# Optimization experiments

Measured on AMD Instinct MI355X. Metric: run time of the kernel, lower is better.

The kernel has to match this reference:

```python
import jax, jax.numpy as jnp
import numpy as np

B, N, DIM, H, DH = 2, 2048, 1024, 16, 64
INNER = H * DH


def _rotate_half(t):
    # interleaved pairs: (..., d) -> rotate each (x1, x2) pair to (-x2, x1)
    t = t.reshape(*t.shape[:-1], -1, 2)
    x1, x2 = t[..., 0], t[..., 1]
    return jnp.stack((-x2, x1), axis=-1).reshape(*t.shape[:-2], -1)


def _apply_rotary(freqs, t):
    # freqs: [B, N, DH] -> broadcast over heads; t: [B, H, N, DH]
    f = freqs[:, None, :, :]
    return t * jnp.cos(f) + _rotate_half(t) * jnp.sin(f)


def _layernorm(x, g, b, eps=1e-5):
    mu = jnp.mean(x, axis=-1, keepdims=True)
    var = jnp.mean((x - mu) ** 2, axis=-1, keepdims=True)
    return (x - mu) * jax.lax.rsqrt(var + eps) * g + b


def setup_inputs() -> dict:
    key = jax.random.key(0)
    ks = jax.random.split(key, 8)
    x = jax.random.normal(ks[0], (B, N, DIM), jnp.float32)
    rotary = jax.random.normal(ks[1], (B, N, DH), jnp.float32)
    ln_g = jnp.ones((DIM,), jnp.float32)
    ln_b = jnp.zeros((DIM,), jnp.float32)
    w_qkv = jax.random.normal(ks[2], (DIM, 3 * INNER), jnp.float32) / np.sqrt(DIM)
    b_qkv = jnp.zeros((3 * INNER,), jnp.float32)
    w_out = jax.random.normal(ks[3], (INNER, DIM), jnp.float32) / np.sqrt(INNER)
    b_out = jnp.zeros((DIM,), jnp.float32)
    return {"x": x, "rotary": rotary, "ln_g": ln_g, "ln_b": ln_b,
            "w_qkv": w_qkv, "b_qkv": b_qkv, "w_out": w_out, "b_out": b_out}


def reference(x, rotary, ln_g, ln_b, w_qkv, b_qkv, w_out, b_out):
    h = _layernorm(x, ln_g, ln_b)
    qkv = h @ w_qkv + b_qkv                      # [B, N, 3*INNER]
    q, k, v = jnp.split(qkv, 3, axis=-1)
    # b n (h d) -> b h n d
    def to_heads(t):
        return t.reshape(B, N, H, DH).transpose(0, 2, 1, 3)
    q, k, v = to_heads(q), to_heads(k), to_heads(v)
    q = _apply_rotary(rotary, q)
    k = _apply_rotary(rotary, k)
    v = _apply_rotary(rotary, v)                 # rotate_value=True
    scale = DH ** (-0.5)
    attn = jnp.einsum('bhnd,bhmd->bhnm', q, k) * scale
    attn = jax.nn.softmax(attn, axis=-1)
    out = jnp.einsum('bhnm,bhmd->bhnd', attn, v)
    out = _apply_rotary(-rotary, out)            # inverse rotation on values
    out = out.transpose(0, 2, 1, 3).reshape(B, N, INNER)
    return out @ w_out + b_out
```

## Files before the change

kernel.cpp:

```cpp
#include <hip/hip_runtime.h>
#include <hip/hip_bf16.h>

typedef _Float16 f16;
typedef __attribute__((ext_vector_type(4))) float f32x4;
typedef __attribute__((ext_vector_type(8))) _Float16 f16x8;
typedef __attribute__((ext_vector_type(4))) _Float16 f16x4;
typedef __attribute__((ext_vector_type(2))) __fp16 hf2;

#define Bv 2
#define Nv 2048
#define DIMv 1024
#define Hv 16
#define DHv 64
#define INNERv 1024
#define QKV3v 3072

__device__ __forceinline__ void gload16(const void* g, void* l) {
  __builtin_amdgcn_global_load_lds(
      (const __attribute__((address_space(1))) void*)g,
      (__attribute__((address_space(3))) void*)l, 16, 0, 0);
}

__global__ __launch_bounds__(256) void ln_kernel(
    const float* __restrict__ x, const float* __restrict__ g,
    const float* __restrict__ bb, f16* __restrict__ h) {
  const int row = blockIdx.x;
  const int t = threadIdx.x;
  const float4 v = reinterpret_cast<const float4*>(x + (size_t)row * DIMv)[t];
  float s = v.x + v.y + v.z + v.w;
  float sq = v.x * v.x + v.y * v.y + v.z * v.z + v.w * v.w;
#pragma unroll
  for (int o = 32; o > 0; o >>= 1) {
    s += __shfl_down(s, o);
    sq += __shfl_down(sq, o);
  }
  __shared__ float red[8];
  __shared__ float musr[2];
  const int wave = t >> 6, lane = t & 63;
  if (lane == 0) { red[wave] = s; red[4 + wave] = sq; }
  __syncthreads();
  if (t == 0) {
    const float S = red[0] + red[1] + red[2] + red[3];
    const float SQ = red[4] + red[5] + red[6] + red[7];
    const float mu = S * (1.0f / DIMv);
    const float var = SQ * (1.0f / DIMv) - mu * mu;
    musr[0] = mu;
    musr[1] = rsqrtf(var + 1e-5f);
  }
  __syncthreads();
  const float mu = musr[0], rs = musr[1];
  const float4 gv = reinterpret_cast<const float4*>(g)[t];
  const float4 bv = reinterpret_cast<const float4*>(bb)[t];
  f16x4 o;
  o.x = (f16)((v.x - mu) * rs * gv.x + bv.x);
  o.y = (f16)((v.y - mu) * rs * gv.y + bv.y);
  o.z = (f16)((v.z - mu) * rs * gv.z + bv.z);
  o.w = (f16)((v.w - mu) * rs * gv.w + bv.w);
  *reinterpret_cast<f16x4*>(&h[(size_t)row * DIMv + t * 4]) = o;
}

__global__ __launch_bounds__(256) void rotcs_kernel(
    const float* __restrict__ rot, float* __restrict__ c,
    float* __restrict__ s, int n) {
  const int i = blockIdx.x * blockDim.x + threadIdx.x;
  if (i < n) {
    const float f = rot[i];
    c[i] = cosf(f);
    s[i] = sinf(f);
  }
}

__global__ __launch_bounds__(256) void transpose_f16(
    const float* __restrict__ W, f16* __restrict__ Wt, int K, int N) {
  __shared__ float tile[64][65];
  const int t = threadIdx.x;
  const int n0 = blockIdx.x * 64, k0 = blockIdx.y * 64;
#pragma unroll
  for (int i = 0; i < 16; ++i) {
    const int idx = t + i * 256;
    const int r = idx >> 6, c = idx & 63;
    tile[r][c] = W[(size_t)(k0 + r) * N + n0 + c];
  }
  __syncthreads();
#pragma unroll
  for (int i = 0; i < 16; ++i) {
    const int idx = t + i * 256;
    const int r = idx >> 6, c = idx & 63;
    Wt[(size_t)(n0 + r) * K + k0 + c] = (f16)tile[c][r];
  }
}

template <int EPI>
__global__ __launch_bounds__(256) void gemm_mfma(
    const f16* __restrict__ A, const f16* __restrict__ Bt,
    const float* __restrict__ bias, void* __restrict__ Cout,
    const float* __restrict__ cs, const float* __restrict__ sn,
    int M, int N, int K) {
  __shared__ __align__(16) f16 Asb[2][128 * 32];
  __shared__ __align__(16) f16 Bsb[2][128 * 32];
  const int t = threadIdx.x;
  const int l = t & 63, w = t >> 6;
  const int wr = w >> 1, wc = w & 1;
  const int row0 = blockIdx.y * 128, col0 = blockIdx.x * 128;

  const int i1 = t, i2 = t + 256;
  const f16* ga1 = &A[(size_t)(row0 + (i1 >> 2)) * K + (i1 & 3) * 8];
  const f16* ga2 = &A[(size_t)(row0 + (i2 >> 2)) * K + (i2 & 3) * 8];
  const f16* gb1 = &Bt[(size_t)(col0 + (i1 >> 2)) * K + (i1 & 3) * 8];
  const f16* gb2 = &Bt[(size_t)(col0 + (i2 >> 2)) * K + (i2 & 3) * 8];
  const int a_off1 = w * 512, a_off2 = w * 512 + 2048;

  const int rl = l & 15, kg = l >> 4;
  const int ar = (wr * 64 + rl) * 32 + kg * 8;
  const int br = (wc * 64 + rl) * 32 + kg * 8;

  const f32x4 zero = {0.f, 0.f, 0.f, 0.f};
  f32x4 acc[4][4];
#pragma unroll
  for (int m = 0; m < 4; ++m)
#pragma unroll
    for (int n = 0; n < 4; ++n) acc[m][n] = zero;

#define GSTAGE(buf, kk)                           \
  {                                               \
    gload16(ga1 + (kk)*32, &Asb[buf][a_off1]);    \
    gload16(ga2 + (kk)*32, &Asb[buf][a_off2]);    \
    gload16(gb1 + (kk)*32, &Bsb[buf][a_off1]);    \
    gload16(gb2 + (kk)*32, &Bsb[buf][a_off2]);    \
  }

  const int nt = K >> 5;
  GSTAGE(0, 0);

  for (int kt = 0; kt < nt; ++kt) {
    const int cur = kt & 1;
    if (kt + 1 < nt) {
      GSTAGE(cur ^ 1, kt + 1);
      asm volatile("s_waitcnt vmcnt(4)" ::: "memory");
    } else {
      asm volatile("s_waitcnt vmcnt(0)" ::: "memory");
    }
    __builtin_amdgcn_s_barrier();
    __builtin_amdgcn_sched_barrier(0);
    f16x8 af[4], bf[4];
#pragma unroll
    for (int m = 0; m < 4; ++m)
      af[m] = *reinterpret_cast<const f16x8*>(&Asb[cur][ar + m * 16 * 32]);
#pragma unroll
    for (int n = 0; n < 4; ++n)
      bf[n] = *reinterpret_cast<const f16x8*>(&Bsb[cur][br + n * 16 * 32]);
#pragma unroll
    for (int m = 0; m < 4; ++m)
#pragma unroll
      for (int n = 0; n < 4; ++n)
        acc[m][n] =
            __builtin_amdgcn_mfma_f32_16x16x32_f16(af[m], bf[n], acc[m][n], 0, 0, 0);
    asm volatile("" ::: "memory");
    __builtin_amdgcn_s_barrier();
    __builtin_amdgcn_sched_barrier(0);
  }
#undef GSTAGE

#pragma unroll
  for (int m = 0; m < 4; ++m) {
#pragma unroll
    for (int n = 0; n < 4; ++n) {
#pragma unroll
      for (int jr = 0; jr < 4; ++jr) {
        const int rg = row0 + wr * 64 + m * 16 + kg * 4 + jr;
        const int cg = col0 + wc * 64 + n * 16 + rl;
        const float v = acc[m][n][jr] + bias[cg];
        if (EPI == 0) {
          ((float*)Cout)[(size_t)rg * N + cg] = v;
        } else {
          const float p = __shfl_xor(v, 1);
          const size_t cb = (size_t)rg * DHv + (cg & 63);
          const float cc = cs[cb], ss = sn[cb];
          const float y = (l & 1) ? (v * cc + p * ss) : (v * cc - p * ss);
          ((f16*)Cout)[(size_t)rg * N + cg] = (f16)y;
        }
      }
    }
  }
}

__global__ __launch_bounds__(256) void transpose_v(
    const f16* __restrict__ qkvf, f16* __restrict__ vT) {
  const int nt = blockIdx.x, hh = blockIdx.y, b = blockIdx.z;
  const int t = threadIdx.x;
  __shared__ __align__(16) f16 tile[64][80];
  const int nl = t >> 3, dc = (t & 7) * 8;
#pragma unroll
  for (int half = 0; half < 2; ++half) {
    const int n = nl + half * 32;
    *reinterpret_cast<f16x8*>(&tile[n][dc]) = *reinterpret_cast<const f16x8*>(
        &qkvf[(size_t)(b * Nv + nt * 64 + n) * QKV3v + 2 * INNERv + hh * DHv + dc]);
  }
  __syncthreads();
  const int c0 = (t & 7) * 8;
  const int kwp = c0 >> 5, kgp = (c0 >> 3) & 3;
#pragma unroll
  for (int half = 0; half < 2; ++half) {
    const int d = (t >> 3) + half * 32;
    union { f16 e[8]; f16x8 v; } uo;
#pragma unroll
    for (int j = 0; j < 8; ++j) {
      const int mk = (j >> 2) & 1, jr = j & 3;
      const int kap = kwp * 32 + mk * 16 + kgp * 4 + jr;
      uo.e[j] = tile[kap][d];
    }
    *reinterpret_cast<f16x8*>(
        &vT[((size_t)((b * Hv + hh) * DHv + d)) * Nv + nt * 64 + c0]) = uo.v;
  }
}

__global__ __launch_bounds__(256, 4) void attn_mfma(
    const f16* __restrict__ qkvf, const f16* __restrict__ vT,
    const float* __restrict__ cs, const float* __restrict__ sn,
    f16* __restrict__ ao) {
  const int wg = blockIdx.x;
  const int swz = (wg & 7) * 128 + (wg >> 3);
  const int qb = swz & 31;
  const int hh = (swz >> 5) & 15;
  const int b = swz >> 9;
  const int t = threadIdx.x, l = t & 63, w = t >> 6;
  const int qw = w >> 1, kw = w & 1;
  const int rl = l & 15, kg = l >> 4;

  __shared__ __align__(16) f16 KsB[2][64 * 64];
  __shared__ __align__(16) f16 VtB[2][64 * 64];
  __shared__ float Lbuf[2][2][32];

  const size_t qrow0 = (size_t)(b * Nv + qb * 64 + qw * 32);
  f16x8 bq[2][2];
#pragma unroll
  for (int nq = 0; nq < 2; ++nq)
#pragma unroll
    for (int ks = 0; ks < 2; ++ks)
      bq[nq][ks] = *reinterpret_cast<const f16x8*>(
          &qkvf[(qrow0 + nq * 16 + rl) * QKV3v + hh * DHv + ks * 32 + kg * 8]);

  const f32x4 zero = {0.f, 0.f, 0.f, 0.f};
  f32x4 o_acc[2][4];
  float l_part[2] = {0.f, 0.f};
#pragma unroll
  for (int nq = 0; nq < 2; ++nq)
#pragma unroll
    for (int m2 = 0; m2 < 4; ++m2) o_acc[nq][m2] = zero;

  const int srow = t >> 3, sc0 = (t & 7) * 8;
  const f16* vtbh = vT + (size_t)((b * Hv + hh) * DHv) * Nv;
  f16x8 kr0, kr1, vr0, vr1;

#define LOADKV(tile)                                                           \
  {                                                                            \
    const size_t kb0 =                                                         \
        (size_t)(b * Nv + (tile)*64 + srow) * QKV3v + INNERv + hh * DHv + sc0; \
    kr0 = *reinterpret_cast<const f16x8*>(&qkvf[kb0]);                         \
    kr1 = *reinterpret_cast<const f16x8*>(&qkvf[kb0 + (size_t)32 * QKV3v]);    \
    const size_t vb0 = (size_t)srow * Nv + (tile)*64 + sc0;                    \
    vr0 = *reinterpret_cast<const f16x8*>(&vtbh[vb0]);                         \
    vr1 = *reinterpret_cast<const f16x8*>(&vtbh[vb0 + (size_t)32 * Nv]);       \
  }
#define STOREKV(buf)                                                           \
  {                                                                            \
    const int r1 = srow + 32;                                                  \
    *reinterpret_cast<f16x8*>(                                                 \
        &KsB[buf][(srow << 6) | (sc0 ^ ((srow & 7) << 3))]) = kr0;             \
    *reinterpret_cast<f16x8*>(                                                 \
        &KsB[buf][(r1 << 6) | (sc0 ^ ((r1 & 7) << 3))]) = kr1;                 \
    *reinterpret_cast<f16x8*>(                                                 \
        &VtB[buf][(srow << 6) | (sc0 ^ ((srow & 7) << 3))]) = vr0;             \
    *reinterpret_cast<f16x8*>(                                                 \
        &VtB[buf][(r1 << 6) | (sc0 ^ ((r1 & 7) << 3))]) = vr1;                 \
  }

  LOADKV(0);
  STOREKV(0);
  LOADKV(1);
  __syncthreads();

  const float SC2 = 0.125f * 1.44269504f;

  for (int kt = 0; kt < 32; ++kt) {
    const int cur = kt & 1;
    const f16* Kc = &KsB[cur][0];
    const f16* Vc = &VtB[cur][0];

    f16x8 ak[2][2];
#pragma unroll
    for (int mk = 0; mk < 2; ++mk)
#pragma unroll
      for (int ks = 0; ks < 2; ++ks)
        ak[mk][ks] = *reinterpret_cast<const f16x8*>(
            &Kc[((kw * 32 + mk * 16 + rl) << 6) |
                ((ks * 32 + kg * 8) ^ ((rl & 7) << 3))]);
    f16x8 av[4];
#pragma unroll
    for (int m2 = 0; m2 < 4; ++m2)
      av[m2] = *reinterpret_cast<const f16x8*>(
          &Vc[((m2 * 16 + rl) << 6) |
              ((kw * 32 + kg * 8) ^ ((rl & 7) << 3))]);

    f32x4 sa[2][2];
#pragma unroll
    for (int mk = 0; mk < 2; ++mk)
#pragma unroll
      for (int nq = 0; nq < 2; ++nq) sa[mk][nq] = zero;
    __builtin_amdgcn_s_setprio(1);
#pragma unroll
    for (int ks = 0; ks < 2; ++ks)
#pragma unroll
      for (int mk = 0; mk < 2; ++mk)
#pragma unroll
        for (int nq = 0; nq < 2; ++nq)
          sa[mk][nq] = __builtin_amdgcn_mfma_f32_16x16x32_f16(
              ak[mk][ks], bq[nq][ks], sa[mk][nq], 0, 0, 0);
    __builtin_amdgcn_s_setprio(0);

    f16x8 pb[2];
#pragma unroll
    for (int nq = 0; nq < 2; ++nq) {
      float p00 = exp2f(fminf(sa[0][nq][0] * SC2, 13.0f));
      float p01 = exp2f(fminf(sa[0][nq][1] * SC2, 13.0f));
      float p02 = exp2f(fminf(sa[0][nq][2] * SC2, 13.0f));
      float p03 = exp2f(fminf(sa[0][nq][3] * SC2, 13.0f));
      float p10 = exp2f(fminf(sa[1][nq][0] * SC2, 13.0f));
      float p11 = exp2f(fminf(sa[1][nq][1] * SC2, 13.0f));
      float p12 = exp2f(fminf(sa[1][nq][2] * SC2, 13.0f));
      float p13 = exp2f(fminf(sa[1][nq][3] * SC2, 13.0f));
      l_part[nq] += ((p00 + p01) + (p02 + p03)) + ((p10 + p11) + (p12 + p13));
      union { hf2 h2[4]; f16x8 v; } u;
      u.h2[0] = __builtin_amdgcn_cvt_pkrtz(p00, p01);
      u.h2[1] = __builtin_amdgcn_cvt_pkrtz(p02, p03);
      u.h2[2] = __builtin_amdgcn_cvt_pkrtz(p10, p11);
      u.h2[3] = __builtin_amdgcn_cvt_pkrtz(p12, p13);
      pb[nq] = u.v;
    }

    __builtin_amdgcn_s_setprio(1);
#pragma unroll
    for (int nq = 0; nq < 2; ++nq)
#pragma unroll
      for (int m2 = 0; m2 < 4; ++m2)
        o_acc[nq][m2] = __builtin_amdgcn_mfma_f32_16x16x32_f16(
            av[m2], pb[nq], o_acc[nq][m2], 0, 0, 0);
    __builtin_amdgcn_s_setprio(0);

    if (kt < 31) STOREKV(1 - cur);
    if (kt < 30) LOADKV(kt + 2);
    __syncthreads();
  }

#pragma unroll
  for (int nq = 0; nq < 2; ++nq) {
    l_part[nq] += __shfl_xor(l_part[nq], 16);
    l_part[nq] += __shfl_xor(l_part[nq], 32);
  }
  if (kg == 0) {
    Lbuf[qw][kw][rl] = l_part[0];
    Lbuf[qw][kw][16 + rl] = l_part[1];
  }
  {
    char* ob = (qw == 0 ? (char*)KsB : (char*)VtB) + kw * 8192;
#pragma unroll
    for (int nq = 0; nq < 2; ++nq)
#pragma unroll
      for (int m2 = 0; m2 < 4; ++m2)
        *reinterpret_cast<f32x4*>(
            ob + (nq * 16 + rl) * 256 +
            ((m2 * 64 + kg * 16) ^ ((rl & 7) << 4))) = o_acc[nq][m2];
  }
  __syncthreads();
  {
    const int q_local = w * 16 + (l >> 2);
    const int qw_r = q_local >> 5, q_in = q_local & 31;
    const int d0 = (l & 3) * 16;
    char* rb = (qw_r == 0 ? (char*)KsB : (char*)VtB);
    const float linv = 1.0f / (Lbuf[qw_r][0][q_in] + Lbuf[qw_r][1][q_in]);
    const size_t nq_g = (size_t)(b * Nv + qb * 64 + q_local);
    const size_t cb = nq_g * DHv + d0;
    union { f16 e[16]; f16x8 v[2]; } uo;
#pragma unroll
    for (int j = 0; j < 4; ++j) {
      const unsigned off = q_in * 256 + (((l & 3) * 64 + j * 16) ^ ((q_in & 7) << 4));
      const f32x4 a = *reinterpret_cast<const f32x4*>(rb + off);
      const f32x4 c2 = *reinterpret_cast<const f32x4*>(rb + 8192 + off);
      const float4 csv = *reinterpret_cast<const float4*>(&cs[cb + j * 4]);
      const float4 snv = *reinterpret_cast<const float4*>(&sn[cb + j * 4]);
      const float o0 = (a[0] + c2[0]) * linv;
      const float o1 = (a[1] + c2[1]) * linv;
      const float o2 = (a[2] + c2[2]) * linv;
      const float o3 = (a[3] + c2[3]) * linv;
      uo.e[j * 4 + 0] = (f16)(o0 * csv.x + o1 * snv.x);
      uo.e[j * 4 + 1] = (f16)(o1 * csv.y - o0 * snv.y);
      uo.e[j * 4 + 2] = (f16)(o2 * csv.z + o3 * snv.z);
      uo.e[j * 4 + 3] = (f16)(o3 * csv.w - o2 * snv.w);
    }
    f16* aop = &ao[nq_g * INNERv + hh * DHv + d0];
    *reinterpret_cast<f16x8*>(aop) = uo.v[0];
    *reinterpret_cast<f16x8*>(aop + 8) = uo.v[1];
  }
#undef LOADKV
#undef STOREKV
}

extern "C" void kernel_launch(void* const* d_in, const int* in_sizes, int n_in,
                              void* d_out, int out_size, void* d_ws, size_t ws_size,
                              hipStream_t stream) {
  (void)in_sizes; (void)n_in; (void)out_size; (void)ws_size;
  const float* x = (const float*)d_in[0];
  const float* rot = (const float*)d_in[1];
  const float* ln_g = (const float*)d_in[2];
  const float* ln_b = (const float*)d_in[3];
  const float* w_qkv = (const float*)d_in[4];
  const float* b_qkv = (const float*)d_in[5];
  const float* w_out = (const float*)d_in[6];
  const float* b_out = (const float*)d_in[7];

  char* p = (char*)d_ws;
  f16* h = (f16*)p;            p += (size_t)Bv * Nv * DIMv * 2;
  float* cs = (float*)p;       p += (size_t)Bv * Nv * DHv * 4;
  float* sn = (float*)p;       p += (size_t)Bv * Nv * DHv * 4;
  f16* wqT = (f16*)p;          p += (size_t)QKV3v * DIMv * 2;
  f16* woT = (f16*)p;          p += (size_t)DIMv * INNERv * 2;
  f16* qkvf = (f16*)p;         p += (size_t)Bv * Nv * QKV3v * 2;
  f16* ao = (f16*)p;           p += (size_t)Bv * Nv * INNERv * 2;
  f16* vT = (f16*)p;           p += (size_t)Bv * Hv * DHv * Nv * 2;

  ln_kernel<<<dim3(Bv * Nv), dim3(256), 0, stream>>>(x, ln_g, ln_b, h);
  rotcs_kernel<<<dim3((Bv * Nv * DHv) / 256), dim3(256), 0, stream>>>(
      rot, cs, sn, Bv * Nv * DHv);
  transpose_f16<<<dim3(QKV3v / 64, DIMv / 64), dim3(256), 0, stream>>>(
      w_qkv, wqT, DIMv, QKV3v);
  transpose_f16<<<dim3(INNERv / 64, DIMv / 64), dim3(256), 0, stream>>>(
      w_out, woT, DIMv, INNERv);
  gemm_mfma<1><<<dim3(QKV3v / 128, (Bv * Nv) / 128), dim3(256), 0, stream>>>(
      h, wqT, b_qkv, (void*)qkvf, cs, sn, Bv * Nv, QKV3v, DIMv);
  transpose_v<<<dim3(Nv / 64, Hv, Bv), dim3(256), 0, stream>>>(qkvf, vT);
  attn_mfma<<<dim3(1024), dim3(256), 0, stream>>>(qkvf, vT, cs, sn, ao);
  gemm_mfma<0><<<dim3(DIMv / 128, (Bv * Nv) / 128), dim3(256), 0, stream>>>(
      ao, woT, b_out, d_out, nullptr, nullptr, Bv * Nv, DIMv, INNERv);
}
```

Measured before the change: 158.3 us.

## Add 256x256-tile 4-stage pipelined MFMA GEMM for QKV projection

```diff
diff --git a/kernel.cpp b/kernel.cpp
--- a/kernel.cpp
+++ b/kernel.cpp
@@ -87,6 +87,129 @@
     const int idx = t + i * 256;
     const int r = idx >> 6, c = idx & 63;
     Wt[(size_t)(n0 + r) * K + k0 + c] = (f16)tile[c][r];
+  }
+}
+
+template <int EPI>
+__global__ __launch_bounds__(512, 2) void gemm_mfma256(
+    const f16* __restrict__ A, const f16* __restrict__ Bt,
+    const float* __restrict__ bias, void* __restrict__ Cout,
+    const float* __restrict__ cs, const float* __restrict__ sn,
+    int M, int N, int K) {
+  __shared__ __align__(16) f16 AsbF[4 * 8192];
+  __shared__ __align__(16) f16 BsbF[4 * 8192];
+  const int t = threadIdx.x;
+  const int l = t & 63, w = t >> 6;
+  const int wm = w >> 2, wn = w & 3;
+  const int row0 = blockIdx.y * 256, col0 = blockIdx.x * 256;
+  const int rl = l & 15, kg = l >> 4;
+
+  const int i0 = t, i1 = t + 512;
+  const int rA0 = i0 >> 2, cח0 = (i0 & 3) ^ ((rA0 >> 1) & 3);
+  const int rA1 = i1 >> 2, cח1 = (i1 & 3) ^ ((rA1 >> 1) & 3);
+  const f16* gA0 = &A[(size_t)(row0 + rA0) * K + cח0 * 8];
+  const f16* gA1 = &A[(size_t)(row0 + rA1) * K + cח1 * 8];
+  const f16* gB0 = &Bt[(size_t)(col0 + rA0) * K + cח0 * 8];
+  const f16* gB1 = &Bt[(size_t)(col0 + rA1) * K + cח1 * 8];
+
+  const f32x4 zero = {0.f, 0.f, 0.f, 0.f};
+  f32x4 acc[8][4];
+#pragma unroll
+  for (int m = 0; m < 8; ++m)
+#pragma unroll
+    for (int n = 0; n < 4; ++n) acc[m][n] = zero;
+
+#define STAGE256(bufi, kk)                                  \
+  {                                                         \
+    gload16(gA0 + (kk) * 32, &AsbF[(bufi)*8192 + i0 * 8]);  \
+    gload16(gA1 + (kk) * 32, &AsbF[(bufi)*8192 + i1 * 8]);  \
+    gload16(gB0 + (kk) * 32, &BsbF[(bufi)*8192 + i0 * 8]);  \
+    gload16(gB1 + (kk) * 32, &BsbF[(bufi)*8192 + i1 * 8]);  \
+  }
+
+  const int nkt = K >> 5;
+  STAGE256(0, 0);
+  STAGE256(1, 1);
+  STAGE256(2, 2);
+
+  for (int kt = 0; kt < nkt; ++kt) {
+    const int buf = kt & 3;
+    const f16* Ab = &AsbF[buf * 8192];
+    const f16* Bb = &BsbF[buf * 8192];
+
+    if (kt + 2 < nkt)
+      asm volatile("s_waitcnt vmcnt(8)" ::: "memory");
+    else if (kt + 1 < nkt)
+      asm volatile("s_waitcnt vmcnt(4)" ::: "memory");
+    else
+      asm volatile("s_waitcnt vmcnt(0)" ::: "memory");
+    __builtin_amdgcn_s_barrier();
+    __builtin_amdgcn_sched_barrier(0);
+
+    f16x8 bfr[4], afr[4];
+#pragma unroll
+    for (int n = 0; n < 4; ++n) {
+      const int rowB = wn * 64 + n * 16 + rl;
+      bfr[n] = *reinterpret_cast<const f16x8*>(
+          &Bb[rowB * 32 + ((kg ^ ((rowB >> 1) & 3)) << 3)]);
+    }
+#pragma unroll
+    for (int m = 0; m < 4; ++m) {
+      const int rowA = wm * 128 + m * 16 + rl;
+      afr[m] = *reinterpret_cast<const f16x8*>(
+          &Ab[rowA * 32 + ((kg ^ ((rowA >> 1) & 3)) << 3)]);
+    }
+    __builtin_amdgcn_s_setprio(1);
+#pragma unroll
+    for (int m = 0; m < 4; ++m)
+#pragma unroll
+      for (int n = 0; n < 4; ++n)
+        acc[m][n] =
+            __builtin_amdgcn_mfma_f32_16x16x32_f16(afr[m], bfr[n], acc[m][n], 0, 0, 0);
+    __builtin_amdgcn_s_setprio(0);
+
+    asm volatile("" ::: "memory");
+    __builtin_amdgcn_s_barrier();
+    __builtin_amdgcn_sched_barrier(0);
+    if (kt + 3 < nkt) STAGE256((kt + 3) & 3, kt + 3);
+#pragma unroll
+    for (int m = 0; m < 4; ++m) {
+      const int rowA = wm * 128 + (m + 4) * 16 + rl;
+      afr[m] = *reinterpret_cast<const f16x8*>(
+          &Ab[rowA * 32 + ((kg ^ ((rowA >> 1) & 3)) << 3)]);
+    }
+    __builtin_amdgcn_s_setprio(1);
+#pragma unroll
+    for (int m = 0; m < 4; ++m)
+#pragma unroll
+      for (int n = 0; n < 4; ++n)
+        acc[m + 4][n] =
+            __builtin_amdgcn_mfma_f32_16x16x32_f16(afr[m], bfr[n], acc[m + 4][n], 0, 0, 0);
+    __builtin_amdgcn_s_setprio(0);
+    asm volatile("" ::: "memory");
+  }
+#undef STAGE256
+
+#pragma unroll
+  for (int m = 0; m < 8; ++m) {
+#pragma unroll
+    for (int n = 0; n < 4; ++n) {
+#pragma unroll
+      for (int jr = 0; jr < 4; ++jr) {
+        const int rg = row0 + wm * 128 + m * 16 + kg * 4 + jr;
+        const int cg = col0 + wn * 64 + n * 16 + rl;
+        const float v = acc[m][n][jr] + bias[cg];
+        if (EPI == 0) {
+          ((float*)Cout)[(size_t)rg * N + cg] = v;
+        } else {
+          const float p = __shfl_xor(v, 1);
+          const size_t cb = (size_t)rg * DHv + (cg & 63);
+          const float cc = cs[cb], ss = sn[cb];
+          const float y = (l & 1) ? (v * cc + p * ss) : (v * cc - p * ss);
+          ((f16*)Cout)[(size_t)rg * N + cg] = (f16)y;
+        }
+      }
+    }
   }
 }
 
@@ -435,7 +558,7 @@
       w_qkv, wqT, DIMv, QKV3v);
   transpose_f16<<<dim3(INNERv / 64, DIMv / 64), dim3(256), 0, stream>>>(
       w_out, woT, DIMv, INNERv);
-  gemm_mfma<1><<<dim3(QKV3v / 128, (Bv * Nv) / 128), dim3(256), 0, stream>>>(
+  gemm_mfma256<1><<<dim3(QKV3v / 256, (Bv * Nv) / 256), dim3(512), 0, stream>>>(
       h, wqT, b_qkv, (void*)qkvf, cs, sn, Bv * Nv, QKV3v, DIMv);
   transpose_v<<<dim3(Nv / 64, Hv, Bv), dim3(256), 0, stream>>>(qkvf, vT);
   attn_mfma<<<dim3(1024), dim3(256), 0, stream>>>(qkvf, vT, cs, sn, ao);
```

Result: no change. 159.3 us (+0.6%).

## Add 256x256 eight-wave MFMA GEMM with swizzled LDS for QKV projection

Applied to the files above, without the earlier changes.

```diff
diff --git a/kernel.cpp b/kernel.cpp
--- a/kernel.cpp
+++ b/kernel.cpp
@@ -87,6 +87,157 @@
     const int idx = t + i * 256;
     const int r = idx >> 6, c = idx & 63;
     Wt[(size_t)(n0 + r) * K + k0 + c] = (f16)tile[c][r];
+  }
+}
+
+template <int EPI>
+__global__ __launch_bounds__(512, 1) void gemm_mfma256(
+    const f16* __restrict__ A, const f16* __restrict__ Bt,
+    const float* __restrict__ bias, void* __restrict__ Cout,
+    const float* __restrict__ cs, const float* __restrict__ sn,
+    int M, int N, int K) {
+  __shared__ __align__(16) f16 Abuf[32768];
+  __shared__ __align__(16) f16 Bbuf[32768];
+  const int t = threadIdx.x, l = t & 63, w = t >> 6;
+  const int wm = w >> 2, wn = w & 3;
+  const int row0 = blockIdx.y * 256, col0 = blockIdx.x * 256;
+  const int rl = l & 15, kg = l >> 4;
+
+  const int r0l = w * 32 + (l >> 2);
+  const int r1l = r0l + 16;
+  const int c0e = (((l & 3) ^ ((r0l & 3) ^ ((r0l >> 2) & 3))) << 3);
+  const int c1e = (((l & 3) ^ ((r1l & 3) ^ ((r1l >> 2) & 3))) << 3);
+  const f16* gA0 = &A[(size_t)(row0 + r0l) * K + c0e];
+  const f16* gA1 = &A[(size_t)(row0 + r1l) * K + c1e];
+  const f16* gB0 = &Bt[(size_t)(col0 + r0l) * K + c0e];
+  const f16* gB1 = &Bt[(size_t)(col0 + r1l) * K + c1e];
+  const int ldsw = w * 1024;
+
+  const f32x4 zero = {0.f, 0.f, 0.f, 0.f};
+  f32x4 acc[8][4];
+#pragma unroll
+  for (int m = 0; m < 8; ++m)
+#pragma unroll
+    for (int n = 0; n < 4; ++n) acc[m][n] = zero;
+
+#define STA(kh, tile)                                                      \
+  {                                                                        \
+    const int db = (((tile)&1) << 14) + ((kh) << 13) + ldsw;               \
+    gload16(gA0 + (size_t)(tile)*64 + (kh)*32, &Abuf[db]);                 \
+    gload16(gA1 + (size_t)(tile)*64 + (kh)*32, &Abuf[db + 512]);           \
+  }
+#define STB(kh, tile)                                                      \
+  {                                                                        \
+    const int db = (((tile)&1) << 14) + ((kh) << 13) + ldsw;               \
+    gload16(gB0 + (size_t)(tile)*64 + (kh)*32, &Bbuf[db]);                 \
+    gload16(gB1 + (size_t)(tile)*64 + (kh)*32, &Bbuf[db + 512]);           \
+  }
+#define RDA(frag, mg, ks, cur)                                             \
+  {                                                                        \
+    const int r = wm * 128 + (mg)*16 + rl;                                 \
+    frag = *reinterpret_cast<const f16x8*>(                                \
+        &Abuf[((cur) << 14) + ((ks) << 13) + r * 32 +                      \
+              ((kg ^ ((r & 3) ^ ((r >> 2) & 3))) << 3)]);                  \
+  }
+#define RDB(frag, n, ks, cur)                                              \
+  {                                                                        \
+    const int r = wn * 64 + (n)*16 + rl;                                   \
+    frag = *reinterpret_cast<const f16x8*>(                                \
+        &Bbuf[((cur) << 14) + ((ks) << 13) + r * 32 +                      \
+              ((kg ^ ((r & 3) ^ ((r >> 2) & 3))) << 3)]);                  \
+  }
+#define MFMA_CLUSTER(mbase, afr, bfr)                                      \
+  {                                                                        \
+    asm volatile("s_waitcnt lgkmcnt(0)" ::: "memory");                     \
+    __builtin_amdgcn_sched_barrier(0);                                     \
+    __builtin_amdgcn_s_setprio(1);                                         \
+    _Pragma("unroll") for (int m = 0; m < 4; ++m)                          \
+        _Pragma("unroll") for (int n = 0; n < 4; ++n) acc[(mbase) + m][n] =\
+        __builtin_amdgcn_mfma_f32_16x16x32_f16(afr[m], bfr[n],             \
+                                               acc[(mbase) + m][n], 0, 0, 0);\
+    __builtin_amdgcn_s_setprio(0);                                         \
+  }
+
+  const int nkt = K >> 6;
+  STA(0, 0); STB(0, 0); STA(1, 0); STB(1, 0);
+  asm volatile("s_waitcnt vmcnt(0)" ::: "memory");
+  __builtin_amdgcn_s_barrier();
+
+  f16x8 af[4], bf[4];
+  for (int kt = 0; kt < nkt; ++kt) {
+    const int cur = kt & 1;
+    const bool pf = (kt + 1 < nkt);
+    if (pf) {
+      STA(0, kt + 1);
+      asm volatile("s_waitcnt vmcnt(6)" ::: "memory");
+    } else {
+      asm volatile("s_waitcnt vmcnt(4)" ::: "memory");
+    }
+    __builtin_amdgcn_s_barrier();
+    __builtin_amdgcn_sched_barrier(0);
+#pragma unroll
+    for (int n = 0; n < 4; ++n) RDB(bf[n], n, 0, cur);
+#pragma unroll
+    for (int m = 0; m < 4; ++m) RDA(af[m], m, 0, cur);
+    MFMA_CLUSTER(0, af, bf);
+    if (pf) {
+      STB(0, kt + 1);
+      asm volatile("s_waitcnt vmcnt(6)" ::: "memory");
+    }
+    __builtin_amdgcn_s_barrier();
+    __builtin_amdgcn_sched_barrier(0);
+#pragma unroll
+    for (int m = 0; m < 4; ++m) RDA(af[m], 4 + m, 0, cur);
+    MFMA_CLUSTER(4, af, bf);
+    if (pf) {
+      STA(1, kt + 1);
+      asm volatile("s_waitcnt vmcnt(6)" ::: "memory");
+    } else {
+      asm volatile("s_waitcnt vmcnt(0)" ::: "memory");
+    }
+    __builtin_amdgcn_s_barrier();
+    __builtin_amdgcn_sched_barrier(0);
+#pragma unroll
+    for (int n = 0; n < 4; ++n) RDB(bf[n], n, 1, cur);
+#pragma unroll
+    for (int m = 0; m < 4; ++m) RDA(af[m], m, 1, cur);
+    MFMA_CLUSTER(0, af, bf);
+    if (pf) {
+      STB(1, kt + 1);
+      asm volatile("s_waitcnt vmcnt(6)" ::: "memory");
+    }
+    __builtin_amdgcn_s_barrier();
+    __builtin_amdgcn_sched_barrier(0);
+#pragma unroll
+    for (int m = 0; m < 4; ++m) RDA(af[m], 4 + m, 1, cur);
+    MFMA_CLUSTER(4, af, bf);
+  }
+#undef STA
+#undef STB
+#undef RDA
+#undef RDB
+#undef MFMA_CLUSTER
+
+#pragma unroll
+  for (int m = 0; m < 8; ++m) {
+#pragma unroll
+    for (int n = 0; n < 4; ++n) {
+#pragma unroll
+      for (int jr = 0; jr < 4; ++jr) {
+        const int rg = row0 + wm * 128 + m * 16 + kg * 4 + jr;
+        const int cg = col0 + wn * 64 + n * 16 + rl;
+        const float v = acc[m][n][jr] + bias[cg];
+        if (EPI == 0) {
+          ((float*)Cout)[(size_t)rg * N + cg] = v;
+        } else {
+          const float p = __shfl_xor(v, 1);
+          const size_t cb = (size_t)rg * DHv + (cg & 63);
+          const float cc = cs[cb], ss = sn[cb];
+          const float y = (l & 1) ? (v * cc + p * ss) : (v * cc - p * ss);
+          ((f16*)Cout)[(size_t)rg * N + cg] = (f16)y;
+        }
+      }
+    }
   }
 }
 
@@ -435,7 +586,7 @@
       w_qkv, wqT, DIMv, QKV3v);
   transpose_f16<<<dim3(INNERv / 64, DIMv / 64), dim3(256), 0, stream>>>(
       w_out, woT, DIMv, INNERv);
-  gemm_mfma<1><<<dim3(QKV3v / 128, (Bv * Nv) / 128), dim3(256), 0, stream>>>(
+  gemm_mfma256<1><<<dim3(QKV3v / 256, (Bv * Nv) / 256), dim3(512), 0, stream>>>(
       h, wqT, b_qkv, (void*)qkvf, cs, sn, Bv * Nv, QKV3v, DIMv);
   transpose_v<<<dim3(Nv / 64, Hv, Bv), dim3(256), 0, stream>>>(qkvf, vT);
   attn_mfma<<<dim3(1024), dim3(256), 0, stream>>>(qkvf, vT, cs, sn, ao);
```

After: 151.8 us. 4.1% less time.

## Stage pre-swizzled K/V tile images into LDS via direct global-to-LDS loads

Applied to the files above, without the earlier changes.

```diff
diff --git a/kernel.cpp b/kernel.cpp
--- a/kernel.cpp
+++ b/kernel.cpp
@@ -101,7 +101,14 @@
   const int t = threadIdx.x;
   const int l = t & 63, w = t >> 6;
   const int wr = w >> 1, wc = w & 1;
-  const int row0 = blockIdx.y * 128, col0 = blockIdx.x * 128;
+
+  const int nwg = gridDim.x;
+  const int wg = blockIdx.x;
+  const int nid = (wg & 7) * (nwg >> 3) + (wg >> 3);
+  const int rows = M >> 7;
+  const int by = nid % rows;
+  const int bx = nid / rows;
+  const int row0 = by * 128, col0 = bx * 128;
 
   const int i1 = t, i2 = t + 256;
   const f16* ga1 = &A[(size_t)(row0 + (i1 >> 2)) * K + (i1 & 3) * 8];
@@ -184,10 +191,23 @@
   }
 }
 
-__global__ __launch_bounds__(256) void transpose_v(
-    const f16* __restrict__ qkvf, f16* __restrict__ vT) {
+__global__ __launch_bounds__(256) void prep_kv(
+    const f16* __restrict__ qkvf, f16* __restrict__ Kimg,
+    f16* __restrict__ Vimg) {
   const int nt = blockIdx.x, hh = blockIdx.y, b = blockIdx.z;
   const int t = threadIdx.x;
+  const size_t tbase = ((size_t)((b * Hv + hh) * 32 + nt)) << 12;
+
+#pragma unroll
+  for (int half = 0; half < 2; ++half) {
+    const int task = t + half * 256;
+    const int key = task >> 3, c = task & 7;
+    const int d = (c * 8) ^ ((key & 7) << 3);
+    const f16x8 kv = *reinterpret_cast<const f16x8*>(
+        &qkvf[(size_t)(b * Nv + nt * 64 + key) * QKV3v + INNERv + hh * DHv + d]);
+    *reinterpret_cast<f16x8*>(&Kimg[tbase + key * 64 + c * 8]) = kv;
+  }
+
   __shared__ __align__(16) f16 tile[64][80];
   const int nl = t >> 3, dc = (t & 7) * 8;
 #pragma unroll
@@ -210,14 +230,14 @@
       uo.e[j] = tile[kap][d];
     }
     *reinterpret_cast<f16x8*>(
-        &vT[((size_t)((b * Hv + hh) * DHv + d)) * Nv + nt * 64 + c0]) = uo.v;
+        &Vimg[tbase + d * 64 + (c0 ^ ((d & 7) << 3))]) = uo.v;
   }
 }
 
 __global__ __launch_bounds__(256, 4) void attn_mfma(
-    const f16* __restrict__ qkvf, const f16* __restrict__ vT,
-    const float* __restrict__ cs, const float* __restrict__ sn,
-    f16* __restrict__ ao) {
+    const f16* __restrict__ qkvf, const f16* __restrict__ Kimg,
+    const f16* __restrict__ Vimg, const float* __restrict__ cs,
+    const float* __restrict__ sn, f16* __restrict__ ao) {
   const int wg = blockIdx.x;
   const int swz = (wg & 7) * 128 + (wg >> 3);
   const int qb = swz & 31;
@@ -227,8 +247,8 @@
   const int qw = w >> 1, kw = w & 1;
   const int rl = l & 15, kg = l >> 4;
 
-  __shared__ __align__(16) f16 KsB[2][64 * 64];
-  __shared__ __align__(16) f16 VtB[2][64 * 64];
+  __shared__ __align__(16) f16 KsB[2][4096];
+  __shared__ __align__(16) f16 VtB[2][4096];
   __shared__ float Lbuf[2][2][32];
 
   const size_t qrow0 = (size_t)(b * Nv + qb * 64 + qw * 32);
@@ -240,50 +260,45 @@
       bq[nq][ks] = *reinterpret_cast<const f16x8*>(
           &qkvf[(qrow0 + nq * 16 + rl) * QKV3v + hh * DHv + ks * 32 + kg * 8]);
 
+  f16x8 ones;
+#pragma unroll
+  for (int j = 0; j < 8; ++j) ones[j] = (f16)1.0f;
+
   const f32x4 zero = {0.f, 0.f, 0.f, 0.f};
   f32x4 o_acc[2][4];
-  float l_part[2] = {0.f, 0.f};
+  f32x4 l_acc[2] = {zero, zero};
 #pragma unroll
   for (int nq = 0; nq < 2; ++nq)
 #pragma unroll
     for (int m2 = 0; m2 < 4; ++m2) o_acc[nq][m2] = zero;
 
-  const int srow = t >> 3, sc0 = (t & 7) * 8;
-  const f16* vtbh = vT + (size_t)((b * Hv + hh) * DHv) * Nv;
-  f16x8 kr0, kr1, vr0, vr1;
-
-#define LOADKV(tile)                                                           \
-  {                                                                            \
-    const size_t kb0 =                                                         \
-        (size_t)(b * Nv + (tile)*64 + srow) * QKV3v + INNERv + hh * DHv + sc0; \
-    kr0 = *reinterpret_cast<const f16x8*>(&qkvf[kb0]);                         \
-    kr1 = *reinterpret_cast<const f16x8*>(&qkvf[kb0 + (size_t)32 * QKV3v]);    \
-    const size_t vb0 = (size_t)srow * Nv + (tile)*64 + sc0;                    \
-    vr0 = *reinterpret_cast<const f16x8*>(&vtbh[vb0]);                         \
-    vr1 = *reinterpret_cast<const f16x8*>(&vtbh[vb0 + (size_t)32 * Nv]);       \
-  }
-#define STOREKV(buf)                                                           \
-  {                                                                            \
-    const int r1 = srow + 32;                                                  \
-    *reinterpret_cast<f16x8*>(                                                 \
-        &KsB[buf][(srow << 6) | (sc0 ^ ((srow & 7) << 3))]) = kr0;             \
-    *reinterpret_cast<f16x8*>(                                                 \
-        &KsB[buf][(r1 << 6) | (sc0 ^ ((r1 & 7) << 3))]) = kr1;                 \
-    *reinterpret_cast<f16x8*>(                                                 \
-        &VtB[buf][(srow << 6) | (sc0 ^ ((srow & 7) << 3))]) = vr0;             \
-    *reinterpret_cast<f16x8*>(                                                 \
-        &VtB[buf][(r1 << 6) | (sc0 ^ ((r1 & 7) << 3))]) = vr1;                 \
-  }
-
-  LOADKV(0);
-  STOREKV(0);
-  LOADKV(1);
-  __syncthreads();
+  const size_t ibase = (((size_t)((b * Hv + hh) * 32)) << 12) + w * 512 + l * 8;
+  const f16* kimg_t = Kimg + ibase;
+  const f16* vimg_t = Vimg + ibase;
+
+#define STAGEI(buf, tile)                                          \
+  {                                                                \
+    gload16(kimg_t + ((tile) << 12), &KsB[buf][w * 512]);          \
+    gload16(kimg_t + ((tile) << 12) + 2048, &KsB[buf][w * 512 + 2048]); \
+    gload16(vimg_t + ((tile) << 12), &VtB[buf][w * 512]);          \
+    gload16(vimg_t + ((tile) << 12) + 2048, &VtB[buf][w * 512 + 2048]); \
+  }
+
+  STAGEI(0, 0);
 
   const float SC2 = 0.125f * 1.44269504f;
 
   for (int kt = 0; kt < 32; ++kt) {
     const int cur = kt & 1;
+    if (kt + 1 < 32) {
+      STAGEI(cur ^ 1, kt + 1);
+      asm volatile("s_waitcnt vmcnt(4)" ::: "memory");
+    } else {
+      asm volatile("s_waitcnt vmcnt(0)" ::: "memory");
+    }
+    __builtin_amdgcn_s_barrier();
+    __builtin_amdgcn_sched_barrier(0);
+
     const f16* Kc = &KsB[cur][0];
     const f16* Vc = &VtB[cur][0];
 
@@ -329,7 +344,6 @@
       float p11 = exp2f(fminf(sa[1][nq][1] * SC2, 13.0f));
       float p12 = exp2f(fminf(sa[1][nq][2] * SC2, 13.0f));
       float p13 = exp2f(fminf(sa[1][nq][3] * SC2, 13.0f));
-      l_part[nq] += ((p00 + p01) + (p02 + p03)) + ((p10 + p11) + (p12 + p13));
       union { hf2 h2[4]; f16x8 v; } u;
       u.h2[0] = __builtin_amdgcn_cvt_pkrtz(p00, p01);
       u.h2[1] = __builtin_amdgcn_cvt_pkrtz(p02, p03);
@@ -341,25 +355,25 @@
     __builtin_amdgcn_s_setprio(1);
 #pragma unroll
     for (int nq = 0; nq < 2; ++nq)
+      l_acc[nq] = __builtin_amdgcn_mfma_f32_16x16x32_f16(
+          ones, pb[nq], l_acc[nq], 0, 0, 0);
+#pragma unroll
+    for (int nq = 0; nq < 2; ++nq)
 #pragma unroll
       for (int m2 = 0; m2 < 4; ++m2)
         o_acc[nq][m2] = __builtin_amdgcn_mfma_f32_16x16x32_f16(
             av[m2], pb[nq], o_acc[nq][m2], 0, 0, 0);
     __builtin_amdgcn_s_setprio(0);
 
-    if (kt < 31) STOREKV(1 - cur);
-    if (kt < 30) LOADKV(kt + 2);
-    __syncthreads();
-  }
-
-#pragma unroll
-  for (int nq = 0; nq < 2; ++nq) {
-    l_part[nq] += __shfl_xor(l_part[nq], 16);
-    l_part[nq] += __shfl_xor(l_part[nq], 32);
-  }
+    asm volatile("" ::: "memory");
+    __builtin_amdgcn_s_barrier();
+    __builtin_amdgcn_sched_barrier(0);
+  }
+#undef STAGEI
+
   if (kg == 0) {
-    Lbuf[qw][kw][rl] = l_part[0];
-    Lbuf[qw][kw][16 + rl] = l_part[1];
+    Lbuf[qw][kw][rl] = l_acc[0][0];
+    Lbuf[qw][kw][16 + rl] = l_acc[1][0];
   }
   {
     char* ob = (qw == 0 ? (char*)KsB : (char*)VtB) + kw * 8192;
@@ -401,8 +415,6 @@
     *reinterpret_cast<f16x8*>(aop) = uo.v[0];
     *reinterpret_cast<f16x8*>(aop + 8) = uo.v[1];
   }
-#undef LOADKV
-#undef STOREKV
 }
 
 extern "C" void kernel_launch(void* const* d_in, const int* in_sizes, int n_in,
@@ -426,7 +438,8 @@
   f16* woT = (f16*)p;          p += (size_t)DIMv * INNERv * 2;
   f16* qkvf = (f16*)p;         p += (size_t)Bv * Nv * QKV3v * 2;
   f16* ao = (f16*)p;           p += (size_t)Bv * Nv * INNERv * 2;
-  f16* vT = (f16*)p;           p += (size_t)Bv * Hv * DHv * Nv * 2;
+  f16* Kimg = (f16*)p;         p += (size_t)Bv * Hv * 32 * 4096 * 2;
+  f16* Vimg = (f16*)p;         p += (size_t)Bv * Hv * 32 * 4096 * 2;
 
   ln_kernel<<<dim3(Bv * Nv), dim3(256), 0, stream>>>(x, ln_g, ln_b, h);
   rotcs_kernel<<<dim3((Bv * Nv * DHv) / 256), dim3(256), 0, stream>>>(
@@ -435,10 +448,10 @@
       w_qkv, wqT, DIMv, QKV3v);
   transpose_f16<<<dim3(INNERv / 64, DIMv / 64), dim3(256), 0, stream>>>(
       w_out, woT, DIMv, INNERv);
-  gemm_mfma<1><<<dim3(QKV3v / 128, (Bv * Nv) / 128), dim3(256), 0, stream>>>(
+  gemm_mfma<1><<<dim3((QKV3v / 128) * ((Bv * Nv) / 128)), dim3(256), 0, stream>>>(
       h, wqT, b_qkv, (void*)qkvf, cs, sn, Bv * Nv, QKV3v, DIMv);
-  transpose_v<<<dim3(Nv / 64, Hv, Bv), dim3(256), 0, stream>>>(qkvf, vT);
-  attn_mfma<<<dim3(1024), dim3(256), 0, stream>>>(qkvf, vT, cs, sn, ao);
-  gemm_mfma<0><<<dim3(DIMv / 128, (Bv * Nv) / 128), dim3(256), 0, stream>>>(
+  prep_kv<<<dim3(Nv / 64, Hv, Bv), dim3(256), 0, stream>>>(qkvf, Kimg, Vimg);
+  attn_mfma<<<dim3(1024), dim3(256), 0, stream>>>(qkvf, Kimg, Vimg, cs, sn, ao);
+  gemm_mfma<0><<<dim3((DIMv / 128) * ((Bv * Nv) / 128)), dim3(256), 0, stream>>>(
       ao, woT, b_out, d_out, nullptr, nullptr, Bv * Nv, DIMv, INNERv);
 }
```

After: 163.9 us. +3.6%, slower.
